# Optimization experiments

Hardware: AMD Instinct MI355X
Metric: run time of the kernel (lower is better)

Reference implementation:

```python
import jax, jax.numpy as jnp
import numpy as np

L, H, D, DH, N, B, V, PAD = 6, 8, 512, 64, 300, 64, 32000, 0
DFF = 4 * D

def _layernorm(x, g, b):
    m = x.mean(-1, keepdims=True)
    v = ((x - m) ** 2).mean(-1, keepdims=True)
    return (x - m) * jax.lax.rsqrt(v + 1e-5) * g + b

def setup_inputs() -> dict:
    key = jax.random.key(0)
    ks = jax.random.split(key, 8)
    emb = jax.random.normal(ks[0], (V, D), dtype=jnp.float32) * 0.02
    emb = emb.at[PAD].set(0.0)  # padding_idx row is zero
    pos = jax.random.normal(ks[1], (N, D), dtype=jnp.float32) * 0.02
    Wk = jax.random.normal(ks[2], (L, H, D, DH), dtype=jnp.float32) * 0.02  # shared K=Q=V proj (module bug: uses self.key for all three)
    Wo = jax.random.normal(ks[3], (L, D, D), dtype=jnp.float32) * 0.02
    W1 = jax.random.normal(ks[4], (L, D, DFF), dtype=jnp.float32) * 0.02
    b1 = jnp.zeros((L, DFF), dtype=jnp.float32)
    W2 = jax.random.normal(ks[5], (L, DFF, D), dtype=jnp.float32) * 0.02
    b2 = jnp.zeros((L, D), dtype=jnp.float32)
    gamma = jnp.ones((L, D), dtype=jnp.float32)   # ONE LayerNorm per block, shared for both norms
    beta = jnp.zeros((L, D), dtype=jnp.float32)
    tokens = jax.random.randint(ks[6], (B, N), 0, V)
    return dict(tokens=tokens, emb=emb, pos=pos, Wk=Wk, Wo=Wo, W1=W1, b1=b1, W2=W2, b2=b2, gamma=gamma, beta=beta)

def reference(tokens, emb, pos, Wk, Wo, W1, b1, W2, b2, gamma, beta):
    x = emb[tokens] + pos[: tokens.shape[1]]  # [B,N,D]
    scale = 1.0 / jnp.sqrt(jnp.asarray(D, x.dtype))  # divides by sqrt(512), NOT sqrt(head_dim)
    for l in range(L):
        k = jnp.einsum('bnd,hde->bhne', x, Wk[l])          # Q=K=V  [B,H,N,DH]
        s = jnp.einsum('bhne,bhme->bhnm', k, k) * scale    # [B,H,N,N]
        a = jax.nn.softmax(s, axis=-1)
        o = jnp.einsum('bhnm,bhme->bhne', a, k)            # [B,H,N,DH]
        o = o.transpose(0, 2, 1, 3).reshape(x.shape[0], x.shape[1], D)
        z = _layernorm(o @ Wo[l] + x, gamma[l], beta[l])
        h = jax.nn.relu(z @ W1[l] + b1[l]) @ W2[l] + b2[l]
        x = _layernorm(h + z, gamma[l], beta[l])
    return x
```

## Files before the change

kernel.cpp:

```cpp
#include <hip/hip_runtime.h>

#define L_LAYERS 6
#define HEADS    8
#define DMODEL   512
#define DHEAD    64
#define SEQ      300
#define BATCH    64
#define DFFN     2048
#define BN_ROWS  (BATCH*SEQ)
#define NPAD     320

typedef __bf16 bf16_t;
typedef bf16_t bf16x8 __attribute__((ext_vector_type(8)));
typedef bf16_t bf16x4 __attribute__((ext_vector_type(4)));
typedef float  f32x4  __attribute__((ext_vector_type(4)));

#define GLOAD16(gp, lp) __builtin_amdgcn_global_load_lds( \
    (__attribute__((address_space(1))) void*)(gp),        \
    (__attribute__((address_space(3))) void*)(lp), 16, 0, 0)

#define MEMBAR() asm volatile("" ::: "memory")
#define PHASE_BAR() do { MEMBAR(); __builtin_amdgcn_s_barrier(); MEMBAR(); } while (0)
#define VMCNT4() asm volatile("s_waitcnt vmcnt(4)" ::: "memory")

__global__ __launch_bounds__(256) void transpose_w8(const float* __restrict__ w,
                                                    bf16_t* __restrict__ o,
                                                    int K, int Nc)
{
    int idx = blockIdx.x * 256 + threadIdx.x;
    int n   = idx % Nc;
    int r   = idx / Nc;
    int k8  = (r % (K / 8)) * 8;
    int l   = r / (K / 8);
    const float* wp = w + (size_t)l * K * Nc + (size_t)k8 * Nc + n;
    bf16x8 t;
#pragma unroll
    for (int j = 0; j < 8; ++j) t[j] = (bf16_t)wp[(size_t)j * Nc];
    *(bf16x8*)(o + (size_t)l * K * Nc + (size_t)n * K + k8) = t;
}

__global__ __launch_bounds__(256) void transpose_wk8(const float* __restrict__ wk,
                                                     bf16_t* __restrict__ o)
{
    int idx = blockIdx.x * 256 + threadIdx.x;
    int e  = idx % DHEAD;
    int r  = idx / DHEAD;
    int d8 = (r % (DMODEL / 8)) * 8;
    r      = r / (DMODEL / 8);
    int h  = r % HEADS;
    int l  = r / HEADS;
    const float* wp = wk + (((size_t)(l * HEADS + h) * DMODEL + d8) * DHEAD + e);
    bf16x8 t;
#pragma unroll
    for (int j = 0; j < 8; ++j) t[j] = (bf16_t)wp[(size_t)j * DHEAD];
    *(bf16x8*)(o + (size_t)l * DMODEL * DMODEL + (size_t)(h * DHEAD + e) * DMODEL + d8) = t;
}

__global__ __launch_bounds__(128) void embed_k(const int* __restrict__ tok,
                                               const float* __restrict__ emb,
                                               const float* __restrict__ pos,
                                               bf16_t* __restrict__ xb)
{
    int row = blockIdx.x;
    int n   = row % SEQ;
    int tkn = tok[row];
    int c   = threadIdx.x * 4;
    float4 e = *(const float4*)(emb + (size_t)tkn * DMODEL + c);
    float4 p = *(const float4*)(pos + (size_t)n * DMODEL + c);
    bf16x4 o;
    o[0] = (bf16_t)(e.x + p.x); o[1] = (bf16_t)(e.y + p.y);
    o[2] = (bf16_t)(e.z + p.z); o[3] = (bf16_t)(e.w + p.w);
    *(bf16x4*)(xb + (size_t)row * DMODEL + c) = o;
}

template <int EPI, typename OUT_T>
__global__ __launch_bounds__(512, 2) void gemm256(const bf16_t* __restrict__ A,
                                                  const bf16_t* __restrict__ BT,
                                                  OUT_T* __restrict__ C,
                                                  const float* __restrict__ bias,
                                                  const bf16_t* __restrict__ resid,
                                                  int K, int Nc, int tiles_n)
{
    __shared__ bf16_t smem[65536];
    bf16_t* As  = smem;
    bf16_t* Bsm = smem + 32768;

    const int t = threadIdx.x;
    const int nwg = gridDim.x;
    const int q = nwg >> 3, r = nwg & 7;
    const int xc = blockIdx.x & 7, sq = blockIdx.x >> 3;
    const int lt = (xc < r ? xc * (q + 1) : r * (q + 1) + (xc - r) * q) + sq;
    const int tm = lt / tiles_n, tn = lt % tiles_n;

    const bf16_t* Ab = A  + (size_t)tm * 256 * K;
    const bf16_t* Bb = BT + (size_t)tn * 256 * K;
    const int lane = t & 63, wid = t >> 6;
    const int wr = wid >> 2, wc = wid & 3;
    const int fr = lane & 15, fq = lane >> 4;
    const int NT = K >> 6;

    auto stage_a = [&](int dbuf, int half, int kt) {
#pragma unroll
        for (int j = 0; j < 2; ++j) {
            int idx8 = (j * 512 + t) * 8;
            int rl   = idx8 >> 6;
            int cg   = (idx8 & 63) ^ ((rl & 7) << 3);
            GLOAD16(Ab + (size_t)(half * 128 + rl) * K + kt * 64 + cg,
                    As + dbuf * 16384 + half * 8192 + idx8);
        }
    };
    auto stage_b = [&](int dbuf, int nq, int kt) {
#pragma unroll
        for (int j = 0; j < 2; ++j) {
            int idx8 = (j * 512 + t) * 8;
            int rl   = idx8 >> 6;
            int cg   = (idx8 & 63) ^ ((rl & 7) << 3);
            int grow = (rl >> 5) * 64 + nq * 32 + (rl & 31);
            GLOAD16(Bb + (size_t)grow * K + kt * 64 + cg,
                    Bsm + dbuf * 16384 + nq * 8192 + idx8);
        }
    };

    const f32x4 FZ = {0.f, 0.f, 0.f, 0.f};
    f32x4 acc[8][4];
#pragma unroll
    for (int m = 0; m < 8; ++m)
#pragma unroll
        for (int n = 0; n < 4; ++n) acc[m][n] = FZ;

    stage_a(0, 0, 0); stage_a(0, 1, 0);
    stage_b(0, 0, 0); stage_b(0, 1, 0);
    stage_b(1, 0, 1);
    VMCNT4();
    PHASE_BAR();

    for (int tt = 0; tt < NT; ++tt) {
        const int buf = tt & 1, nbuf = buf ^ 1;
        const bf16_t* Ap = As + buf * 16384 + (wr * 128 + fr) * 64;
#pragma unroll
        for (int ph = 0; ph < 4; ++ph) {
            const int nq = ph >> 1, kk = ph & 1;
            const int ca = (kk * 32 + fq * 8) ^ ((fr & 7) << 3);
            bf16x8 af[8];
#pragma unroll
            for (int m = 0; m < 8; ++m)
                af[m] = *(const bf16x8*)(Ap + m * 1024 + ca);
            const bf16_t* Bp = Bsm + buf * 16384 + nq * 8192 + (wc * 32 + fr) * 64;
            bf16x8 b0 = *(const bf16x8*)(Bp + ca);
            bf16x8 b1 = *(const bf16x8*)(Bp + 1024 + ca);

            if (ph == 0) { if (tt + 1 < NT) stage_a(nbuf, 0, tt + 1); }
            if (ph == 1) { if (tt + 1 < NT) stage_a(nbuf, 1, tt + 1); VMCNT4(); }
            if (ph == 2) { if (tt + 2 < NT) stage_b(buf, 0, tt + 2); }
            if (ph == 3) { if (tt + 1 < NT) stage_b(nbuf, 1, tt + 1); VMCNT4(); }

            PHASE_BAR();
            __builtin_amdgcn_s_setprio(1);
#pragma unroll
            for (int m = 0; m < 8; ++m) {
                acc[m][nq * 2]     = __builtin_amdgcn_mfma_f32_16x16x32_bf16(af[m], b0, acc[m][nq * 2], 0, 0, 0);
                acc[m][nq * 2 + 1] = __builtin_amdgcn_mfma_f32_16x16x32_bf16(af[m], b1, acc[m][nq * 2 + 1], 0, 0, 0);
            }
            __builtin_amdgcn_s_setprio(0);
            PHASE_BAR();
        }
    }

#pragma unroll
    for (int m = 0; m < 8; ++m) {
        const int rowg = tm * 256 + wr * 128 + m * 16 + fq * 4;
#pragma unroll
        for (int n = 0; n < 4; ++n) {
            const int colg = tn * 256 + wc * 64 + n * 16 + fr;
            float bv = (EPI == 2 || EPI == 3) ? bias[colg] : 0.f;
#pragma unroll
            for (int rr = 0; rr < 4; ++rr) {
                float v = acc[m][n][rr] + bv;
                if (EPI == 2) v = fmaxf(v, 0.f);
                if (EPI == 1 || EPI == 3) v += (float)resid[(size_t)(rowg + rr) * Nc + colg];
                C[(size_t)(rowg + rr) * Nc + colg] = (OUT_T)v;
            }
        }
    }
}

__global__ __launch_bounds__(256) void attn_k(const bf16_t* __restrict__ kin,
                                              bf16_t* __restrict__ out)
{
    __shared__ bf16_t Kl[NPAD * 64];
    __shared__ bf16_t KT[64 * NPAD];
    __shared__ bf16_t Pl[4 * 16 * NPAD];

    const int bh = blockIdx.x;
    const int b  = bh >> 3, h = bh & 7;
    const bf16_t* kbase = kin + (size_t)b * SEQ * DMODEL + h * DHEAD;
    const int t  = threadIdx.x;
    const int rr = t >> 3;
    const int cg = (t & 7) * 8;

    for (int pass = 0; pass < NPAD / 32; ++pass) {
        int row = pass * 32 + rr;
        bf16x8 v;
        if (row < SEQ) v = *(const bf16x8*)(kbase + (size_t)row * DMODEL + cg);
        else {
#pragma unroll
            for (int j = 0; j < 8; ++j) v[j] = (bf16_t)0.f;
        }
        *(bf16x8*)(Kl + row * 64 + (cg ^ ((row & 7) << 3))) = v;
#pragma unroll
        for (int j = 0; j < 8; ++j) {
            int col = cg + j;
            KT[col * NPAD + (row ^ ((col & 7) << 3))] = v[j];
        }
    }
    __syncthreads();

    const int lane = t & 63, w = t >> 6;
    const int fr = lane & 15, fq = lane >> 4;
    const float scale = 0.044194173824159216f;
    const f32x4 FZ = {0.f, 0.f, 0.f, 0.f};

    for (int i = 0; i < 5; ++i) {
        int qt = w * 5 + i;
        f32x4 s[20];
#pragma unroll
        for (int ct = 0; ct < 20; ++ct) s[ct] = FZ;
#pragma unroll
        for (int kk = 0; kk < 2; ++kk) {
            int qrow = qt * 16 + fr;
            bf16x8 aq = *(const bf16x8*)(Kl + qrow * 64 + ((kk * 32 + fq * 8) ^ ((qrow & 7) << 3)));
#pragma unroll
            for (int ct = 0; ct < 20; ++ct) {
                int krow = ct * 16 + fr;
                bf16x8 bk = *(const bf16x8*)(Kl + krow * 64 + ((kk * 32 + fq * 8) ^ ((krow & 7) << 3)));
                s[ct] = __builtin_amdgcn_mfma_f32_16x16x32_bf16(aq, bk, s[ct], 0, 0, 0);
            }
        }
#pragma unroll
        for (int r = 0; r < 4; ++r) {
            float mx = -1e30f;
#pragma unroll
            for (int ct = 0; ct < 20; ++ct) {
                float v = s[ct][r] * scale;
                if (ct * 16 + fr < SEQ) mx = fmaxf(mx, v);
            }
            mx = fmaxf(mx, __shfl_xor(mx, 1));
            mx = fmaxf(mx, __shfl_xor(mx, 2));
            mx = fmaxf(mx, __shfl_xor(mx, 4));
            mx = fmaxf(mx, __shfl_xor(mx, 8));
            float p[20];
            float sm = 0.f;
#pragma unroll
            for (int ct = 0; ct < 20; ++ct) {
                float v = (ct * 16 + fr < SEQ) ? __expf(s[ct][r] * scale - mx) : 0.f;
                p[ct] = v; sm += v;
            }
            sm += __shfl_xor(sm, 1); sm += __shfl_xor(sm, 2);
            sm += __shfl_xor(sm, 4); sm += __shfl_xor(sm, 8);
            float rinv = 1.f / sm;
            int pr = fq * 4 + r;
#pragma unroll
            for (int ct = 0; ct < 20; ++ct) {
                int col = ct * 16 + fr;
                Pl[(w * 16 + pr) * NPAD + (col ^ ((pr & 7) << 3))] = (bf16_t)(p[ct] * rinv);
            }
        }
#pragma unroll
        for (int n = 0; n < 4; ++n) {
            f32x4 oacc = FZ;
#pragma unroll
            for (int kk = 0; kk < 10; ++kk) {
                bf16x8 ap = *(const bf16x8*)(Pl + (w * 16 + fr) * NPAD + ((kk * 32 + fq * 8) ^ ((fr & 7) << 3)));
                int dr = n * 16 + fr;
                bf16x8 bv = *(const bf16x8*)(KT + dr * NPAD + ((kk * 32 + fq * 8) ^ ((dr & 7) << 3)));
                oacc = __builtin_amdgcn_mfma_f32_16x16x32_bf16(ap, bv, oacc, 0, 0, 0);
            }
#pragma unroll
            for (int r = 0; r < 4; ++r) {
                int qrow = qt * 16 + fq * 4 + r;
                if (qrow < SEQ)
                    out[(size_t)(b * SEQ + qrow) * DMODEL + h * DHEAD + n * 16 + fr] = (bf16_t)oacc[r];
            }
        }
    }
}

template <bool FINAL>
__global__ __launch_bounds__(256) void ln_k(const float* __restrict__ in,
                                            const float* __restrict__ gam,
                                            const float* __restrict__ bet,
                                            bf16_t* __restrict__ outb,
                                            float* __restrict__ outf)
{
    int row  = blockIdx.x * 4 + (threadIdx.x >> 6);
    int lane = threadIdx.x & 63;
    const float* x = in + (size_t)row * DMODEL + lane * 8;
    float4 v0 = *(const float4*)x;
    float4 v1 = *(const float4*)(x + 4);
    float s  = v0.x + v0.y + v0.z + v0.w + v1.x + v1.y + v1.z + v1.w;
    float s2 = v0.x * v0.x + v0.y * v0.y + v0.z * v0.z + v0.w * v0.w
             + v1.x * v1.x + v1.y * v1.y + v1.z * v1.z + v1.w * v1.w;
#pragma unroll
    for (int m = 1; m < 64; m <<= 1) { s += __shfl_xor(s, m); s2 += __shfl_xor(s2, m); }
    float mean = s * (1.f / DMODEL);
    float rstd = rsqrtf(s2 * (1.f / DMODEL) - mean * mean + 1e-5f);
    float4 g0 = *(const float4*)(gam + lane * 8), g1 = *(const float4*)(gam + lane * 8 + 4);
    float4 b0 = *(const float4*)(bet + lane * 8), b1 = *(const float4*)(bet + lane * 8 + 4);
    float y[8];
    y[0] = (v0.x - mean) * rstd * g0.x + b0.x;
    y[1] = (v0.y - mean) * rstd * g0.y + b0.y;
    y[2] = (v0.z - mean) * rstd * g0.z + b0.z;
    y[3] = (v0.w - mean) * rstd * g0.w + b0.w;
    y[4] = (v1.x - mean) * rstd * g1.x + b1.x;
    y[5] = (v1.y - mean) * rstd * g1.y + b1.y;
    y[6] = (v1.z - mean) * rstd * g1.z + b1.z;
    y[7] = (v1.w - mean) * rstd * g1.w + b1.w;
    bf16x8 ob;
#pragma unroll
    for (int j = 0; j < 8; ++j) ob[j] = (bf16_t)y[j];
    *(bf16x8*)(outb + (size_t)row * DMODEL + lane * 8) = ob;
    if (FINAL) {
        float4 o0 = {y[0], y[1], y[2], y[3]};
        float4 o1 = {y[4], y[5], y[6], y[7]};
        *(float4*)(outf + (size_t)row * DMODEL + lane * 8)     = o0;
        *(float4*)(outf + (size_t)row * DMODEL + lane * 8 + 4) = o1;
    }
}

extern "C" void kernel_launch(void* const* d_in, const int* in_sizes, int n_in,
                              void* d_out, int out_size, void* d_ws, size_t ws_size,
                              hipStream_t stream)
{
    const int*   tok = (const int*)d_in[0];
    const float* emb = (const float*)d_in[1];
    const float* pos = (const float*)d_in[2];
    const float* Wk  = (const float*)d_in[3];
    const float* Wo  = (const float*)d_in[4];
    const float* W1  = (const float*)d_in[5];
    const float* b1  = (const float*)d_in[6];
    const float* W2  = (const float*)d_in[7];
    const float* b2  = (const float*)d_in[8];
    const float* gam = (const float*)d_in[9];
    const float* bet = (const float*)d_in[10];
    float* outp = (float*)d_out;

    char* ws = (char*)d_ws;
    size_t off = 0;
    auto alloc = [&](size_t bytes) {
        off = (off + 255) & ~(size_t)255;
        void* p = ws + off;
        off += bytes;
        return p;
    };
    bf16_t* WKT  = (bf16_t*)alloc((size_t)L_LAYERS * DMODEL * DMODEL * 2);
    bf16_t* WOT  = (bf16_t*)alloc((size_t)L_LAYERS * DMODEL * DMODEL * 2);
    bf16_t* W1T  = (bf16_t*)alloc((size_t)L_LAYERS * DMODEL * DFFN * 2);
    bf16_t* W2T  = (bf16_t*)alloc((size_t)L_LAYERS * DMODEL * DFFN * 2);
    bf16_t* buf0 = (bf16_t*)alloc((size_t)BN_ROWS * DMODEL * 2);
    bf16_t* buf1 = (bf16_t*)alloc((size_t)BN_ROWS * DMODEL * 2);
    bf16_t* kb   = (bf16_t*)alloc((size_t)BN_ROWS * DMODEL * 2);
    bf16_t* ob   = (bf16_t*)alloc((size_t)BN_ROWS * DMODEL * 2);
    bf16_t* h1b  = (bf16_t*)alloc((size_t)BN_ROWS * DFFN * 2);
    float*  tf   = (float*)alloc((size_t)BN_ROWS * DMODEL * 4);

    transpose_wk8<<<768, 256, 0, stream>>>(Wk, WKT);
    transpose_w8<<<768, 256, 0, stream>>>(Wo, WOT, DMODEL, DMODEL);
    transpose_w8<<<3072, 256, 0, stream>>>(W1, W1T, DMODEL, DFFN);
    transpose_w8<<<3072, 256, 0, stream>>>(W2, W2T, DFFN, DMODEL);

    embed_k<<<BN_ROWS, 128, 0, stream>>>(tok, emb, pos, buf0);

    for (int l = 0; l < L_LAYERS; ++l) {
        gemm256<0, bf16_t><<<75 * 2, 512, 0, stream>>>(
            buf0, WKT + (size_t)l * DMODEL * DMODEL, kb, nullptr, nullptr,
            DMODEL, DMODEL, 2);
        attn_k<<<BATCH * HEADS, 256, 0, stream>>>(kb, ob);
        gemm256<1, float><<<75 * 2, 512, 0, stream>>>(
            ob, WOT + (size_t)l * DMODEL * DMODEL, tf, nullptr, buf0,
            DMODEL, DMODEL, 2);
        ln_k<false><<<BN_ROWS / 4, 256, 0, stream>>>(
            tf, gam + l * DMODEL, bet + l * DMODEL, buf1, nullptr);
        gemm256<2, bf16_t><<<75 * 8, 512, 0, stream>>>(
            buf1, W1T + (size_t)l * DMODEL * DFFN, h1b, b1 + l * DFFN, nullptr,
            DMODEL, DFFN, 8);
        gemm256<3, float><<<75 * 2, 512, 0, stream>>>(
            h1b, W2T + (size_t)l * DMODEL * DFFN, tf, b2 + l * DMODEL, buf1,
            DFFN, DMODEL, 2);
        if (l < L_LAYERS - 1)
            ln_k<false><<<BN_ROWS / 4, 256, 0, stream>>>(
                tf, gam + l * DMODEL, bet + l * DMODEL, buf0, nullptr);
        else
            ln_k<true><<<BN_ROWS / 4, 256, 0, stream>>>(
                tf, gam + l * DMODEL, bet + l * DMODEL, buf0, outp);
    }
}
```

Baseline: 1.692 ms.

## Add 128x128 GEMM for N=512 projections and restructure 256 GEMM phases

Adds a gemm128 kernel (256 threads, 128x128 tiles, double-buffered global_load_lds staging) and uses it for the K-projection, output projection and FFN down-projection, raising the grid from 150 to 600 workgroups to fill the GPU's CUs. The gemm256 main loop is rewritten to load A fragments once per k-half and reuse them across both N quarters, with fewer barriers per tile. The smaller tiles reduce per-block data reuse. The new kernel waits on vmcnt(0) every iteration, which may expose load latency.

After: 1.567 ms. 1.08x faster.

```diff
diff --git a/kernel.cpp b/kernel.cpp
--- a/kernel.cpp
+++ b/kernel.cpp
@@ -22,6 +22,7 @@
 #define MEMBAR() asm volatile("" ::: "memory")
 #define PHASE_BAR() do { MEMBAR(); __builtin_amdgcn_s_barrier(); MEMBAR(); } while (0)
 #define VMCNT4() asm volatile("s_waitcnt vmcnt(4)" ::: "memory")
+#define VMCNT0() asm volatile("s_waitcnt vmcnt(0)" ::: "memory")
 
 __global__ __launch_bounds__(256) void transpose_w8(const float* __restrict__ w,
                                                     bf16_t* __restrict__ o,
@@ -128,42 +129,71 @@
 #pragma unroll
         for (int n = 0; n < 4; ++n) acc[m][n] = FZ;
 
-    stage_a(0, 0, 0); stage_a(0, 1, 0);
-    stage_b(0, 0, 0); stage_b(0, 1, 0);
-    stage_b(1, 0, 1);
+    stage_a(0, 0, 0); stage_a(0, 1, 0); stage_b(0, 0, 0);
+    stage_b(0, 1, 0); stage_b(1, 0, 1);
     VMCNT4();
     PHASE_BAR();
 
     for (int tt = 0; tt < NT; ++tt) {
         const int buf = tt & 1, nbuf = buf ^ 1;
-        const bf16_t* Ap = As + buf * 16384 + (wr * 128 + fr) * 64;
-#pragma unroll
-        for (int ph = 0; ph < 4; ++ph) {
-            const int nq = ph >> 1, kk = ph & 1;
-            const int ca = (kk * 32 + fq * 8) ^ ((fr & 7) << 3);
-            bf16x8 af[8];
-#pragma unroll
-            for (int m = 0; m < 8; ++m)
-                af[m] = *(const bf16x8*)(Ap + m * 1024 + ca);
-            const bf16_t* Bp = Bsm + buf * 16384 + nq * 8192 + (wc * 32 + fr) * 64;
-            bf16x8 b0 = *(const bf16x8*)(Bp + ca);
-            bf16x8 b1 = *(const bf16x8*)(Bp + 1024 + ca);
-
-            if (ph == 0) { if (tt + 1 < NT) stage_a(nbuf, 0, tt + 1); }
-            if (ph == 1) { if (tt + 1 < NT) stage_a(nbuf, 1, tt + 1); VMCNT4(); }
-            if (ph == 2) { if (tt + 2 < NT) stage_b(buf, 0, tt + 2); }
-            if (ph == 3) { if (tt + 1 < NT) stage_b(nbuf, 1, tt + 1); VMCNT4(); }
-
-            PHASE_BAR();
-            __builtin_amdgcn_s_setprio(1);
-#pragma unroll
-            for (int m = 0; m < 8; ++m) {
-                acc[m][nq * 2]     = __builtin_amdgcn_mfma_f32_16x16x32_bf16(af[m], b0, acc[m][nq * 2], 0, 0, 0);
-                acc[m][nq * 2 + 1] = __builtin_amdgcn_mfma_f32_16x16x32_bf16(af[m], b1, acc[m][nq * 2 + 1], 0, 0, 0);
-            }
-            __builtin_amdgcn_s_setprio(0);
-            PHASE_BAR();
-        }
+        const bf16_t* Ap  = As  + buf * 16384 + (wr * 128 + fr) * 64;
+        const bf16_t* Bp0 = Bsm + buf * 16384 + (wc * 32 + fr) * 64;
+        const bf16_t* Bp1 = Bp0 + 8192;
+        const int ca0 = (fq * 8) ^ ((fr & 7) << 3);
+        const int ca1 = ca0 ^ 32;
+        bf16x8 af[8], b0, b1;
+
+#pragma unroll
+        for (int m = 0; m < 8; ++m) af[m] = *(const bf16x8*)(Ap + m * 1024 + ca0);
+        b0 = *(const bf16x8*)(Bp0 + ca0);
+        b1 = *(const bf16x8*)(Bp0 + 1024 + ca0);
+        if (tt + 1 < NT) { stage_a(nbuf, 0, tt + 1); VMCNT4(); }
+        PHASE_BAR();
+        __builtin_amdgcn_s_setprio(1);
+#pragma unroll
+        for (int m = 0; m < 8; ++m) {
+            acc[m][0] = __builtin_amdgcn_mfma_f32_16x16x32_bf16(af[m], b0, acc[m][0], 0, 0, 0);
+            acc[m][1] = __builtin_amdgcn_mfma_f32_16x16x32_bf16(af[m], b1, acc[m][1], 0, 0, 0);
+        }
+        __builtin_amdgcn_s_setprio(0);
+
+        b0 = *(const bf16x8*)(Bp1 + ca0);
+        b1 = *(const bf16x8*)(Bp1 + 1024 + ca0);
+        if (tt + 1 < NT) stage_a(nbuf, 1, tt + 1);
+        __builtin_amdgcn_s_setprio(1);
+#pragma unroll
+        for (int m = 0; m < 8; ++m) {
+            acc[m][2] = __builtin_amdgcn_mfma_f32_16x16x32_bf16(af[m], b0, acc[m][2], 0, 0, 0);
+            acc[m][3] = __builtin_amdgcn_mfma_f32_16x16x32_bf16(af[m], b1, acc[m][3], 0, 0, 0);
+        }
+        __builtin_amdgcn_s_setprio(0);
+
+#pragma unroll
+        for (int m = 0; m < 8; ++m) af[m] = *(const bf16x8*)(Ap + m * 1024 + ca1);
+        b0 = *(const bf16x8*)(Bp0 + ca1);
+        b1 = *(const bf16x8*)(Bp0 + 1024 + ca1);
+        if (tt + 1 < NT) stage_b(nbuf, 1, tt + 1);
+        __builtin_amdgcn_s_setprio(1);
+#pragma unroll
+        for (int m = 0; m < 8; ++m) {
+            acc[m][0] = __builtin_amdgcn_mfma_f32_16x16x32_bf16(af[m], b0, acc[m][0], 0, 0, 0);
+            acc[m][1] = __builtin_amdgcn_mfma_f32_16x16x32_bf16(af[m], b1, acc[m][1], 0, 0, 0);
+        }
+        __builtin_amdgcn_s_setprio(0);
+        PHASE_BAR();
+
+        b0 = *(const bf16x8*)(Bp1 + ca1);
+        b1 = *(const bf16x8*)(Bp1 + 1024 + ca1);
+        if (tt + 2 < NT) stage_b(buf, 0, tt + 2);
+        __builtin_amdgcn_s_setprio(1);
+#pragma unroll
+        for (int m = 0; m < 8; ++m) {
+            acc[m][2] = __builtin_amdgcn_mfma_f32_16x16x32_bf16(af[m], b0, acc[m][2], 0, 0, 0);
+            acc[m][3] = __builtin_amdgcn_mfma_f32_16x16x32_bf16(af[m], b1, acc[m][3], 0, 0, 0);
+        }
+        __builtin_amdgcn_s_setprio(0);
+        if (tt + 2 < NT) { VMCNT4(); } else { VMCNT0(); }
+        PHASE_BAR();
     }
 
 #pragma unroll
@@ -179,6 +209,103 @@
                 if (EPI == 2) v = fmaxf(v, 0.f);
                 if (EPI == 1 || EPI == 3) v += (float)resid[(size_t)(rowg + rr) * Nc + colg];
                 C[(size_t)(rowg + rr) * Nc + colg] = (OUT_T)v;
+            }
+        }
+    }
+}
+
+template <int EPI, typename OUT_T>
+__global__ __launch_bounds__(256, 2) void gemm128(const bf16_t* __restrict__ A,
+                                                  const bf16_t* __restrict__ BT,
+                                                  OUT_T* __restrict__ C,
+                                                  const float* __restrict__ bias,
+                                                  const bf16_t* __restrict__ resid,
+                                                  int K, int Nc, int tiles_n)
+{
+    __shared__ bf16_t smem[32768];
+    bf16_t* As = smem;
+    bf16_t* Bs = smem + 16384;
+
+    const int t = threadIdx.x;
+    const int nwg = gridDim.x;
+    const int q = nwg >> 3, r = nwg & 7;
+    const int xc = blockIdx.x & 7, sq = blockIdx.x >> 3;
+    const int lt = (xc < r ? xc * (q + 1) : r * (q + 1) + (xc - r) * q) + sq;
+    const int tm = lt / tiles_n, tn = lt % tiles_n;
+
+    const bf16_t* Ab = A  + (size_t)tm * 128 * K;
+    const bf16_t* Bb = BT + (size_t)tn * 128 * K;
+    const int lane = t & 63, wid = t >> 6;
+    const int wr = wid >> 1, wc = wid & 1;
+    const int fr = lane & 15, fq = lane >> 4;
+    const int NT = K >> 6;
+
+    auto stage = [&](bf16_t* dst, const bf16_t* src, int kt) {
+#pragma unroll
+        for (int j = 0; j < 4; ++j) {
+            int idx8 = (j * 256 + t) * 8;
+            int rl   = idx8 >> 6;
+            int cg   = (idx8 & 63) ^ ((rl & 7) << 3);
+            GLOAD16(src + (size_t)rl * K + kt * 64 + cg, dst + idx8);
+        }
+    };
+
+    const f32x4 FZ = {0.f, 0.f, 0.f, 0.f};
+    f32x4 acc[4][4];
+#pragma unroll
+    for (int m = 0; m < 4; ++m)
+#pragma unroll
+        for (int n = 0; n < 4; ++n) acc[m][n] = FZ;
+
+    stage(As, Ab, 0); stage(Bs, Bb, 0);
+    VMCNT0(); PHASE_BAR();
+
+    for (int tt = 0; tt < NT; ++tt) {
+        const int buf = tt & 1, nbuf = buf ^ 1;
+        const bf16_t* Ap = As + buf * 8192 + (wr * 64 + fr) * 64;
+        const bf16_t* Bp = Bs + buf * 8192 + (wc * 64 + fr) * 64;
+        const int ca0 = (fq * 8) ^ ((fr & 7) << 3);
+        const int ca1 = ca0 ^ 32;
+        bf16x8 af[4], bfr[4];
+#pragma unroll
+        for (int m = 0; m < 4; ++m) af[m] = *(const bf16x8*)(Ap + m * 1024 + ca0);
+#pragma unroll
+        for (int n = 0; n < 4; ++n) bfr[n] = *(const bf16x8*)(Bp + n * 1024 + ca0);
+        if (tt + 1 < NT) { stage(As + nbuf * 8192, Ab, tt + 1); stage(Bs + nbuf * 8192, Bb, tt + 1); }
+        __builtin_amdgcn_s_setprio(1);
+#pragma unroll
+        for (int m = 0; m < 4; ++m)
+#pragma unroll
+            for (int n = 0; n < 4; ++n)
+                acc[m][n] = __builtin_amdgcn_mfma_f32_16x16x32_bf16(af[m], bfr[n], acc[m][n], 0, 0, 0);
+        __builtin_amdgcn_s_setprio(0);
+#pragma unroll
+        for (int m = 0; m < 4; ++m) af[m] = *(const bf16x8*)(Ap + m * 1024 + ca1);
+#pragma unroll
+        for (int n = 0; n < 4; ++n) bfr[n] = *(const bf16x8*)(Bp + n * 1024 + ca1);
+        __builtin_amdgcn_s_setprio(1);
+#pragma unroll
+        for (int m = 0; m < 4; ++m)
+#pragma unroll
+            for (int n = 0; n < 4; ++n)
+                acc[m][n] = __builtin_amdgcn_mfma_f32_16x16x32_bf16(af[m], bfr[n], acc[m][n], 0, 0, 0);
+        __builtin_amdgcn_s_setprio(0);
+        VMCNT0(); PHASE_BAR();
+    }
+
+#pragma unroll
+    for (int m = 0; m < 4; ++m) {
+#pragma unroll
+        for (int n = 0; n < 4; ++n) {
+            int colg = tn * 128 + wc * 64 + n * 16 + fr;
+            float bv = (EPI == 2 || EPI == 3) ? bias[colg] : 0.f;
+#pragma unroll
+            for (int rr2 = 0; rr2 < 4; ++rr2) {
+                int rowg = tm * 128 + wr * 64 + m * 16 + fq * 4 + rr2;
+                float v = acc[m][n][rr2] + bv;
+                if (EPI == 2) v = fmaxf(v, 0.f);
+                if (EPI == 1 || EPI == 3) v += (float)resid[(size_t)rowg * Nc + colg];
+                C[(size_t)rowg * Nc + colg] = (OUT_T)v;
             }
         }
     }
@@ -371,21 +498,21 @@
     embed_k<<<BN_ROWS, 128, 0, stream>>>(tok, emb, pos, buf0);
 
     for (int l = 0; l < L_LAYERS; ++l) {
-        gemm256<0, bf16_t><<<75 * 2, 512, 0, stream>>>(
+        gemm128<0, bf16_t><<<600, 256, 0, stream>>>(
             buf0, WKT + (size_t)l * DMODEL * DMODEL, kb, nullptr, nullptr,
-            DMODEL, DMODEL, 2);
+            DMODEL, DMODEL, 4);
         attn_k<<<BATCH * HEADS, 256, 0, stream>>>(kb, ob);
-        gemm256<1, float><<<75 * 2, 512, 0, stream>>>(
+        gemm128<1, float><<<600, 256, 0, stream>>>(
             ob, WOT + (size_t)l * DMODEL * DMODEL, tf, nullptr, buf0,
-            DMODEL, DMODEL, 2);
+            DMODEL, DMODEL, 4);
         ln_k<false><<<BN_ROWS / 4, 256, 0, stream>>>(
             tf, gam + l * DMODEL, bet + l * DMODEL, buf1, nullptr);
-        gemm256<2, bf16_t><<<75 * 8, 512, 0, stream>>>(
+        gemm256<2, bf16_t><<<600, 512, 0, stream>>>(
             buf1, W1T + (size_t)l * DMODEL * DFFN, h1b, b1 + l * DFFN, nullptr,
             DMODEL, DFFN, 8);
-        gemm256<3, float><<<75 * 2, 512, 0, stream>>>(
+        gemm128<3, float><<<600, 256, 0, stream>>>(
             h1b, W2T + (size_t)l * DMODEL * DFFN, tf, b2 + l * DMODEL, buf1,
-            DFFN, DMODEL, 2);
+            DFFN, DMODEL, 4);
         if (l < L_LAYERS - 1)
             ln_k<false><<<BN_ROWS / 4, 256, 0, stream>>>(
                 tf, gam + l * DMODEL, bet + l * DMODEL, buf0, nullptr);
```
